# Kernel tuning notes

Hardware: AMD Instinct MI355X
Metric: run time of the kernel (lower is better)

The kernel has to match this reference:

```python
import jax, jax.numpy as jnp
import numpy as np

N, E, H, G = 50000, 500000, 64, 64


def _ln(x, g, b):
    m = jnp.mean(x, -1, keepdims=True)
    v = jnp.var(x, -1, keepdims=True)
    return (x - m) * jax.lax.rsqrt(v + 1e-5) * g + b


def _mlp_ln(x, w1, b1, w2, b2, g, be):
    # Linear -> ReLU -> (Dropout eval no-op) -> Linear -> LayerNorm
    h = jax.nn.relu(x @ w1 + b1)
    return _ln(h @ w2 + b2, g, be)


def setup_inputs() -> dict:
    key = jax.random.key(0)
    ks = jax.random.split(key, 24)
    w = lambda i, s: jax.random.normal(ks[i], s, dtype=jnp.float32) * 0.1
    z = lambda s: jnp.zeros(s, jnp.float32)
    o = lambda s: jnp.ones(s, jnp.float32)
    inp = {
        'x': jax.random.normal(ks[0], (N, 3), dtype=jnp.float32),
        'edge_index': jax.random.randint(ks[1], (2, E), 0, N),
        'edge_attr': jax.random.normal(ks[2], (E, 3), dtype=jnp.float32),
        'batch': jnp.sort(jax.random.randint(ks[3], (N,), 0, G)),
        'ne_w1': w(4, (3, H)), 'ne_b1': z((H,)), 'ne_w2': w(5, (H, H)), 'ne_b2': z((H,)), 'ne_g': o((H,)), 'ne_be': z((H,)),
        'ee_w1': w(6, (3, H)), 'ee_b1': z((H,)), 'ee_w2': w(7, (H, H)), 'ee_b2': z((H,)), 'ee_g': o((H,)), 'ee_be': z((H,)),
        'gin0_eps': z((1,)), 'gin0_w1': w(8, (H, H)), 'gin0_b1': z((H,)), 'gin0_w2': w(9, (H, H)), 'gin0_b2': z((H,)), 'gin0_g': o((H,)), 'gin0_be': z((H,)),
        'gin1_eps': z((1,)), 'gin1_w1': w(10, (H, H)), 'gin1_b1': z((H,)), 'gin1_w2': w(11, (H, H)), 'gin1_b2': z((H,)), 'gin1_g': o((H,)), 'gin1_be': z((H,)),
        'gp_w': w(12, (H, H)), 'gp_b': z((H,)), 'gp_g': o((H,)), 'gp_be': z((H,)),
        'ep_w1': w(13, (4 * H, 2 * H)), 'ep_b1': z((2 * H,)),
        'ep_w2': w(14, (2 * H, H)), 'ep_b2': z((H,)),
        'ep_w3': w(15, (H, 1)), 'ep_b3': z((1,)),
    }
    return inp


def reference(x, edge_index, edge_attr, batch,
              ne_w1, ne_b1, ne_w2, ne_b2, ne_g, ne_be,
              ee_w1, ee_b1, ee_w2, ee_b2, ee_g, ee_be,
              gin0_eps, gin0_w1, gin0_b1, gin0_w2, gin0_b2, gin0_g, gin0_be,
              gin1_eps, gin1_w1, gin1_b1, gin1_w2, gin1_b2, gin1_g, gin1_be,
              gp_w, gp_b, gp_g, gp_be,
              ep_w1, ep_b1, ep_w2, ep_b2, ep_w3, ep_b3):
    src, dst = edge_index[0], edge_index[1]
    # encoders
    h = _mlp_ln(x, ne_w1, ne_b1, ne_w2, ne_b2, ne_g, ne_be)            # [N, H]
    ef = _mlp_ln(edge_attr, ee_w1, ee_b1, ee_w2, ee_b2, ee_g, ee_be)   # [E, H]
    # GINEConv layer 0: mlp((1+eps)*x + scatter_add(relu(x_src + e)))
    msg = jax.nn.relu(h[src] + ef)
    aggr = jnp.zeros_like(h).at[dst].add(msg)
    h = _mlp_ln((1.0 + gin0_eps) * h + aggr, gin0_w1, gin0_b1, gin0_w2, gin0_b2, gin0_g, gin0_be)
    h = jax.nn.relu(h)  # inter-layer activation (dropout eval no-op)
    # GINEConv layer 1
    msg = jax.nn.relu(h[src] + ef)
    aggr = jnp.zeros_like(h).at[dst].add(msg)
    h = _mlp_ln((1.0 + gin1_eps) * h + aggr, gin1_w1, gin1_b1, gin1_w2, gin1_b2, gin1_g, gin1_be)
    # global mean pool over graphs
    seg = jax.ops.segment_sum(h, batch, num_segments=G)                            # [G, H]
    cnt = jax.ops.segment_sum(jnp.ones((h.shape[0], 1), h.dtype), batch, num_segments=G)
    gp = seg / jnp.maximum(cnt, 1.0)
    gf = _ln(jax.nn.relu(gp @ gp_w + gp_b), gp_g, gp_be)                           # [G, H]
    # edge predictor on [src | dst | global | edge] = [E, 4H]
    c = jnp.concatenate([h[src], h[dst], gf[batch[src]], ef], axis=-1)
    t = jnp.tanh(c @ ep_w1 + ep_b1)
    t = jnp.tanh(t @ ep_w2 + ep_b2)
    return jax.nn.sigmoid(t @ ep_w3 + ep_b3)  # [E, 1]
```

## Files before the change

### kernel.cpp

```cpp
#include <hip/hip_runtime.h>
#include <hip/hip_bf16.h>

typedef unsigned int uint;
typedef unsigned short ushort;
typedef __attribute__((ext_vector_type(8))) short short8;
typedef __attribute__((ext_vector_type(4))) float floatx4;

__device__ __forceinline__ float bf2f(ushort u) { return __uint_as_float(((uint)u) << 16); }
__device__ __forceinline__ ushort f2bf(float f) {
  uint u = __float_as_uint(f);
  u += 0x7fffu + ((u >> 16) & 1u);
  return (ushort)(u >> 16);
}
__device__ __forceinline__ uint pk2(float a, float b) {
  return (uint)f2bf(a) | ((uint)f2bf(b) << 16);
}
__device__ __forceinline__ float ldf(const void* p, long i, int m) {
  if (m) return bf2f(((const ushort*)p)[i]);
  return ((const float*)p)[i];
}
__device__ __forceinline__ int get_md(const uint* mdp) {
  return (mdp[0] == 0x3F800000u) ? 0 : 1;
}
__device__ __forceinline__ float fast_rcp(float x) { return __builtin_amdgcn_rcpf(x); }
__device__ __forceinline__ float tanh_fast(float x) {
  float e = __builtin_amdgcn_exp2f(2.8853900818f * x);
  return fmaf(-2.f, fast_rcp(1.f + e), 1.f);
}
__device__ __forceinline__ float sigmoid_fast(float x) {
  float e = __builtin_amdgcn_exp2f(-1.4426950409f * x);
  return fast_rcp(1.f + e);
}

__global__ __launch_bounds__(256) void k_enc_mfma(
    const void* __restrict__ in, int R,
    const void* __restrict__ w1, const void* __restrict__ b1,
    const ushort* __restrict__ w2sw_, const void* __restrict__ b2,
    const void* __restrict__ gam, const void* __restrict__ bet,
    ushort* __restrict__ outp, ushort* __restrict__ outp2,
    const int* __restrict__ epos, const uint* __restrict__ mdp)
{
  __shared__ float xs[64*3];
  __shared__ float w1s[192], b1s[64], b2s[64], gs[64], bs2[64];
  __shared__ __align__(16) ushort T_s[64 * 72];
  int md = get_md(mdp);
  int tid = threadIdx.x;
  long e0 = (long)blockIdx.x * 64;
  if (tid < 192) {
    w1s[tid] = ldf(w1, tid, md);
    int row = tid / 3, cc = tid - row*3;
    long e = e0 + row;
    xs[tid] = (e < R) ? ldf(in, e*3 + cc, md) : 0.f;
  }
  if (tid < 64) { b1s[tid] = ldf(b1, tid, md); b2s[tid] = ldf(b2, tid, md);
                  gs[tid] = ldf(gam, tid, md); bs2[tid] = ldf(bet, tid, md); }
  __syncthreads();
  int lane = tid & 63, wv = tid >> 6;
  int quad = lane >> 4, mm = lane & 15;
  float x0 = xs[(wv*16 + mm)*3 + 0];
  float x1 = xs[(wv*16 + mm)*3 + 1];
  float x2 = xs[(wv*16 + mm)*3 + 2];
  short8 af[2];
#pragma unroll
  for (int s = 0; s < 2; ++s) {
#pragma unroll
    for (int j = 0; j < 8; ++j) {
      int f = s*32 + quad*8 + j;
      float hv = fmaxf(b1s[f] + x0*w1s[f] + x1*w1s[64+f] + x2*w1s[128+f], 0.f);
      af[s][j] = (short)f2bf(hv);
    }
  }
  floatx4 acc[4] = {};
  const short8* Bp = (const short8*)w2sw_;
#pragma unroll
  for (int s = 0; s < 2; ++s) {
#pragma unroll
    for (int t = 0; t < 4; ++t) {
      short8 b = Bp[(s*4 + t)*64 + lane];
      acc[t] = __builtin_amdgcn_mfma_f32_16x16x32_bf16(af[s], b, acc[t], 0, 0, 0);
    }
  }
  float vv[4][4];
#pragma unroll
  for (int t = 0; t < 4; ++t) {
    float bb = b2s[mm + 16*t];
#pragma unroll
    for (int r = 0; r < 4; ++r) vv[t][r] = acc[t][r] + bb;
  }
  float mr[4], vr[4];
#pragma unroll
  for (int r = 0; r < 4; ++r) {
    float s = vv[0][r] + vv[1][r] + vv[2][r] + vv[3][r];
#pragma unroll
    for (int off = 1; off < 16; off <<= 1) s += __shfl_xor(s, off);
    mr[r] = s * 0.015625f;
    float q = 0.f;
#pragma unroll
    for (int t = 0; t < 4; ++t) { float d = vv[t][r] - mr[r]; q = fmaf(d, d, q); }
#pragma unroll
    for (int off = 1; off < 16; off <<= 1) q += __shfl_xor(q, off);
    vr[r] = rsqrtf(q * 0.015625f + 1e-5f);
  }
#pragma unroll
  for (int t = 0; t < 4; ++t) {
    int col = mm + 16*t;
    float g = gs[col], be = bs2[col];
#pragma unroll
    for (int r = 0; r < 4; ++r)
      T_s[(wv*16 + quad*4 + r)*72 + col] = f2bf((vv[t][r] - mr[r]) * vr[r] * g + be);
  }
  __syncthreads();
#pragma unroll
  for (int i = 0; i < 2; ++i) {
    int gi = tid + 256*i;
    int row = gi >> 3, c = gi & 7;
    long e = e0 + row;
    if (e < R) {
      uint4 v = *(const uint4*)&T_s[row*72 + c*8];
      ((uint4*)(outp + e*64))[c] = v;
      if (outp2)
        ((uint4*)(outp2 + (long)epos[e]*64))[c] = v;
    }
  }
}

__global__ __launch_bounds__(256) void k_swz(
    const void* __restrict__ w1, const void* __restrict__ w2,
    const void* __restrict__ w2e, const void* __restrict__ w2n,
    const void* __restrict__ gw10, const void* __restrict__ gw20,
    const void* __restrict__ gw11, const void* __restrict__ gw21,
    ushort* __restrict__ w1sw, ushort* __restrict__ w2sw,
    ushort* __restrict__ ew2sw, ushort* __restrict__ nw2sw,
    ushort* __restrict__ g0w1sw, ushort* __restrict__ g0w2sw,
    ushort* __restrict__ g1w1sw, ushort* __restrict__ g1w2sw,
    int* __restrict__ deg, float* __restrict__ gsum, int Nn,
    const uint* __restrict__ mdp)
{
  int md = get_md(mdp);
  int i = blockIdx.x * 256 + threadIdx.x;
  int nthr = gridDim.x * 256;
  for (int k = i; k < Nn; k += nthr) deg[k] = 0;
  for (int k = i; k < 64*64 + 64; k += nthr) gsum[k] = 0.f;
  if (i < 32768) {
    int q = i & 7, lane = (i >> 3) & 63, tt = (i >> 9) & 7, s = i >> 12;
    int k = s*32 + (lane >> 4)*8 + q, n = (lane & 15) + 16*tt;
    w1sw[i] = f2bf(ldf(w1, k*128 + n, md));
  }
  if (i < 8192) {
    int q = i & 7, lane = (i >> 3) & 63, tt = (i >> 9) & 3, s = i >> 11;
    int k = s*32 + (lane >> 4)*8 + q, n = (lane & 15) + 16*tt;
    int src = k*64 + n;
    w2sw[i]   = f2bf(ldf(w2,   src, md));
    ew2sw[i]  = f2bf(ldf(w2e,  src, md));
    nw2sw[i]  = f2bf(ldf(w2n,  src, md));
    g0w1sw[i] = f2bf(ldf(gw10, src, md));
    g0w2sw[i] = f2bf(ldf(gw20, src, md));
    g1w1sw[i] = f2bf(ldf(gw11, src, md));
    g1w2sw[i] = f2bf(ldf(gw21, src, md));
  }
}

__global__ __launch_bounds__(256) void k_deg(
    const int* __restrict__ ei, int* __restrict__ deg, int E_)
{
  int e = blockIdx.x * 256 + threadIdx.x;
  if (e < E_) atomicAdd(&deg[ei[E_ + e]], 1);
}

__global__ __launch_bounds__(256) void k_scan1(
    const int* __restrict__ deg, int* __restrict__ rs, int* __restrict__ bsum, int Nn)
{
  __shared__ int ls[256];
  int tid = threadIdx.x;
  int i = blockIdx.x * 256 + tid;
  int v = (i < Nn) ? deg[i] : 0;
  ls[tid] = v;
  __syncthreads();
  for (int off = 1; off < 256; off <<= 1) {
    int t = (tid >= off) ? ls[tid - off] : 0;
    __syncthreads();
    ls[tid] += t;
    __syncthreads();
  }
  if (i < Nn) rs[i] = ls[tid] - v;
  if (tid == 255) bsum[blockIdx.x] = ls[255];
}

__global__ __launch_bounds__(256) void k_scan2(
    int* __restrict__ bsum, int nb, int* __restrict__ rs, int Nn)
{
  __shared__ int ls[256];
  int tid = threadIdx.x;
  int chunk = (nb + 255) / 256;
  int c0 = tid * chunk, c1 = min(c0 + chunk, nb);
  int sum = 0;
  for (int i = c0; i < c1; ++i) sum += bsum[i];
  ls[tid] = sum;
  __syncthreads();
  for (int off = 1; off < 256; off <<= 1) {
    int t = (tid >= off) ? ls[tid - off] : 0;
    __syncthreads();
    ls[tid] += t;
    __syncthreads();
  }
  int run = ls[tid] - sum;
  for (int i = c0; i < c1; ++i) { int d = bsum[i]; bsum[i] = run; run += d; }
  if (tid == 255) rs[Nn] = ls[255];
}

__global__ __launch_bounds__(256) void k_scan3(
    int* __restrict__ rs, int* __restrict__ cur,
    const int* __restrict__ bsum, int Nn)
{
  int i = blockIdx.x * 256 + threadIdx.x;
  if (i < Nn) {
    int v = rs[i] + bsum[blockIdx.x];
    rs[i] = v;
    cur[i] = v;
  }
}

__global__ __launch_bounds__(256) void k_fill(
    const int* __restrict__ ei, int* __restrict__ cur,
    int2* __restrict__ ep, int* __restrict__ epos, int E_)
{
  int e = blockIdx.x * 256 + threadIdx.x;
  if (e < E_) {
    int s = ei[e];
    int d = ei[E_ + e];
    int p = atomicAdd(&cur[d], 1);
    ep[p] = make_int2(e, s);
    epos[e] = p;
  }
}

__global__ __launch_bounds__(256) void k_aggr(
    const ushort* __restrict__ hbu, const ushort* __restrict__ efp,
    const int2* __restrict__ ep, const int* __restrict__ rs,
    float* __restrict__ aggr, int Nn)
{
  int gw = (blockIdx.x * 256 + threadIdx.x) >> 6;
  int j = threadIdx.x & 63;
  if (gw >= Nn) return;
  int s0 = rs[gw], s1 = rs[gw + 1];
  float acc = 0.f;
  int idx = s0;
  for (; idx + 2 <= s1; idx += 2) {
    int2 a = ep[idx];
    int2 b = ep[idx + 1];
    float fA = bf2f(efp[(long)idx*64 + j]);
    float fB = bf2f(efp[(long)(idx+1)*64 + j]);
    float hA = bf2f(hbu[(long)a.y*64 + j]);
    float hB = bf2f(hbu[(long)b.y*64 + j]);
    acc += fmaxf(hA + fA, 0.f) + fmaxf(hB + fB, 0.f);
  }
  if (idx < s1) {
    int2 a = ep[idx];
    acc += fmaxf(bf2f(hbu[(long)a.y*64 + j]) + bf2f(efp[(long)idx*64 + j]), 0.f);
  }
  aggr[(long)gw*64 + j] = acc;
}

__global__ __launch_bounds__(256) void k_gine_mfma(
    const ushort* __restrict__ hbin, const float* __restrict__ aggr, int Nn,
    const void* __restrict__ epsp,
    const ushort* __restrict__ w1sw_, const void* __restrict__ b1,
    const ushort* __restrict__ w2sw_, const void* __restrict__ b2,
    const void* __restrict__ gam, const void* __restrict__ bet,
    ushort* __restrict__ hbout, int post_relu, const uint* __restrict__ mdp)
{
  __shared__ __align__(16) ushort Ws1[4096], Ws2[4096];
  __shared__ __align__(16) ushort T_s[64 * 72];
  __shared__ float b1s[64], b2s[64], gs[64], bs2[64];
  int md = get_md(mdp);
  int tid = threadIdx.x;
  {
    const uint4* p1 = (const uint4*)w1sw_;
    const uint4* p2 = (const uint4*)w2sw_;
    ((uint4*)Ws1)[tid] = p1[tid];
    ((uint4*)Ws1)[tid + 256] = p1[tid + 256];
    ((uint4*)Ws2)[tid] = p2[tid];
    ((uint4*)Ws2)[tid + 256] = p2[tid + 256];
  }
  if (tid < 64) { b1s[tid] = ldf(b1, tid, md); b2s[tid] = ldf(b2, tid, md);
                  gs[tid] = ldf(gam, tid, md); bs2[tid] = ldf(bet, tid, md); }
  float ope = 1.f + ldf(epsp, 0, md);
  int lane = tid & 63, wv = tid >> 6;
  int quad = lane >> 4, mm = lane & 15;
  long node = (long)blockIdx.x * 64 + wv*16 + mm;
  long nc = (node < Nn) ? node : (long)(Nn - 1);
  const ushort* hrow = hbin + nc*64;
  const float*  arow = aggr + nc*64;
  short8 af[2];
#pragma unroll
  for (int s = 0; s < 2; ++s) {
    int c = s*4 + quad;
    short8 hv = *(const short8*)(hrow + c*8);
    float4 a0 = *(const float4*)(arow + c*8);
    float4 a1 = *(const float4*)(arow + c*8 + 4);
    float uu[8];
    uu[0] = fmaf(bf2f((ushort)hv[0]), ope, a0.x);
    uu[1] = fmaf(bf2f((ushort)hv[1]), ope, a0.y);
    uu[2] = fmaf(bf2f((ushort)hv[2]), ope, a0.z);
    uu[3] = fmaf(bf2f((ushort)hv[3]), ope, a0.w);
    uu[4] = fmaf(bf2f((ushort)hv[4]), ope, a1.x);
    uu[5] = fmaf(bf2f((ushort)hv[5]), ope, a1.y);
    uu[6] = fmaf(bf2f((ushort)hv[6]), ope, a1.z);
    uu[7] = fmaf(bf2f((ushort)hv[7]), ope, a1.w);
#pragma unroll
    for (int j = 0; j < 8; ++j) af[s][j] = (short)f2bf(uu[j]);
  }
  __syncthreads();
  floatx4 acc[4] = {};
#pragma unroll
  for (int s = 0; s < 2; ++s) {
#pragma unroll
    for (int t = 0; t < 4; ++t) {
      short8 b = *(const short8*)&Ws1[((s*4 + t)*64 + lane)*8];
      acc[t] = __builtin_amdgcn_mfma_f32_16x16x32_bf16(af[s], b, acc[t], 0, 0, 0);
    }
  }
#pragma unroll
  for (int t = 0; t < 4; ++t) {
    int col = mm + 16*t;
    float bb = b1s[col];
#pragma unroll
    for (int r = 0; r < 4; ++r)
      T_s[(wv*16 + quad*4 + r)*72 + col] = f2bf(fmaxf(acc[t][r] + bb, 0.f));
  }
  __syncthreads();
  short8 af2[2];
#pragma unroll
  for (int s = 0; s < 2; ++s)
    af2[s] = *(const short8*)&T_s[(wv*16 + mm)*72 + s*32 + quad*8];
  floatx4 acc2[4] = {};
#pragma unroll
  for (int s = 0; s < 2; ++s) {
#pragma unroll
    for (int t = 0; t < 4; ++t) {
      short8 b = *(const short8*)&Ws2[((s*4 + t)*64 + lane)*8];
      acc2[t] = __builtin_amdgcn_mfma_f32_16x16x32_bf16(af2[s], b, acc2[t], 0, 0, 0);
    }
  }
  float vv[4][4];
#pragma unroll
  for (int t = 0; t < 4; ++t) {
    float bb = b2s[mm + 16*t];
#pragma unroll
    for (int r = 0; r < 4; ++r) vv[t][r] = acc2[t][r] + bb;
  }
  float mr[4], vr[4];
#pragma unroll
  for (int r = 0; r < 4; ++r) {
    float s = vv[0][r] + vv[1][r] + vv[2][r] + vv[3][r];
#pragma unroll
    for (int off = 1; off < 16; off <<= 1) s += __shfl_xor(s, off);
    mr[r] = s * 0.015625f;
    float q = 0.f;
#pragma unroll
    for (int t = 0; t < 4; ++t) { float d = vv[t][r] - mr[r]; q = fmaf(d, d, q); }
#pragma unroll
    for (int off = 1; off < 16; off <<= 1) q += __shfl_xor(q, off);
    vr[r] = rsqrtf(q * 0.015625f + 1e-5f);
  }
  __syncthreads();
#pragma unroll
  for (int t = 0; t < 4; ++t) {
    int col = mm + 16*t;
    float g = gs[col], be = bs2[col];
#pragma unroll
    for (int r = 0; r < 4; ++r) {
      float o = (vv[t][r] - mr[r]) * vr[r] * g + be;
      if (post_relu) o = fmaxf(o, 0.f);
      T_s[(wv*16 + quad*4 + r)*72 + col] = f2bf(o);
    }
  }
  __syncthreads();
#pragma unroll
  for (int i = 0; i < 2; ++i) {
    int gi = tid + 256*i;
    int row = gi >> 3, c = gi & 7;
    long n2 = (long)blockIdx.x * 64 + row;
    if (n2 < Nn)
      ((uint4*)(hbout + n2*64))[c] = *(const uint4*)&T_s[row*72 + c*8];
  }
}

__global__ __launch_bounds__(256) void k_pool_f(
    const ushort* __restrict__ hbu, const int* __restrict__ batch,
    float* __restrict__ gsum, float* __restrict__ gcnt, int Nn)
{
  int gw = (blockIdx.x * 256 + threadIdx.x) >> 6;
  int j = threadIdx.x & 63;
  long r0 = (long)gw * 64;
  if (r0 >= Nn) return;
  long rend = min(r0 + 64, (long)Nn);
  float acc = 0.f; int cur = batch[r0]; int run = 0;
  for (long r = r0; r < rend; ++r) {
    int g = batch[r];
    if (g != cur) {
      atomicAdd(&gsum[cur*64 + j], acc);
      if (j == 0) atomicAdd(&gcnt[cur], (float)run);
      acc = 0.f; run = 0; cur = g;
    }
    acc += bf2f(hbu[r*64 + j]);
    run++;
  }
  atomicAdd(&gsum[cur*64 + j], acc);
  if (j == 0) atomicAdd(&gcnt[cur], (float)run);
}

__global__ __launch_bounds__(64) void k_pool_fin_f(
    const float* __restrict__ gsum, const float* __restrict__ gcnt,
    const void* __restrict__ gpw, const void* __restrict__ gpb,
    const void* __restrict__ gpg, const void* __restrict__ gpbe,
    ushort* __restrict__ gfb, const uint* __restrict__ mdp)
{
  __shared__ float wgs[4096];
  __shared__ float us[64];
  int md = get_md(mdp);
  int j = threadIdx.x;
  int g = blockIdx.x;
  for (int i = j; i < 4096; i += 64) wgs[i] = ldf(gpw, i, md);
  float ic = 1.f / fmaxf(gcnt[g], 1.f);
  us[j] = gsum[g*64 + j] * ic;
  __syncthreads();
  float t = ldf(gpb, j, md);
#pragma unroll
  for (int k = 0; k < 64; ++k) t = fmaf(us[k], wgs[k*64 + j], t);
  t = fmaxf(t, 0.f);
  float m = t;
#pragma unroll
  for (int off = 1; off < 64; off <<= 1) m += __shfl_xor(m, off);
  m *= 0.015625f;
  float d = t - m;
  float v = d * d;
#pragma unroll
  for (int off = 1; off < 64; off <<= 1) v += __shfl_xor(v, off);
  float rs = rsqrtf(v * 0.015625f + 1e-5f);
  gfb[g*64 + j] = f2bf(d * rs * ldf(gpg, j, md) + ldf(gpbe, j, md));
}

__global__ __launch_bounds__(256) void k_pred_mfma(
    const ushort* __restrict__ hb, const ushort* __restrict__ efu,
    const ushort* __restrict__ gfb, const int* __restrict__ ei,
    const int* __restrict__ batch,
    const ushort* __restrict__ w1sw, const ushort* __restrict__ w2sw,
    const void* __restrict__ pb1, const void* __restrict__ pb2,
    const void* __restrict__ pw3, const void* __restrict__ pb3,
    void* __restrict__ out, int E_, const uint* __restrict__ mdp)
{
  __shared__ __align__(16) ushort Ws[8192];
  __shared__ __align__(16) ushort T_s[64 * 136];
  __shared__ float b1s[128], b2s[64], w3s[64];
  int md = get_md(mdp);
  int tid = threadIdx.x;
  if (tid < 128) b1s[tid] = ldf(pb1, tid, md);
  if (tid < 64) { b2s[tid] = ldf(pb2, tid, md); w3s[tid] = ldf(pw3, tid, md); }
  long e0 = (long)blockIdx.x * 64;
  int lane = tid & 63, wv = tid >> 6;
  int quad = lane >> 4, mm = lane & 15;
  long e = e0 + wv*16 + mm;
  if (e >= E_) e = E_ - 1;
  int si = ei[e];
  int di = ei[E_ + e];
  int gi = batch[si];
  const short8* hsrc = (const short8*)(hb  + (long)si*64);
  const short8* hdst = (const short8*)(hb  + (long)di*64);
  const short8* gsrc = (const short8*)(gfb + (long)gi*64);
  const short8* esrc = (const short8*)(efu + e*64);
  short8 af[8];
  af[0] = hsrc[quad]; af[1] = hsrc[4 + quad];
  af[2] = hdst[quad]; af[3] = hdst[4 + quad];
  af[4] = gsrc[quad]; af[5] = gsrc[4 + quad];
  af[6] = esrc[quad]; af[7] = esrc[4 + quad];
  floatx4 acc[8] = {};
  for (int q = 0; q < 4; ++q) {
    __syncthreads();
    const uint4* wp = (const uint4*)(w1sw + q*8192);
#pragma unroll
    for (int i = 0; i < 4; ++i)
      ((uint4*)Ws)[tid + 256*i] = wp[tid + 256*i];
    __syncthreads();
#pragma unroll
    for (int s4 = 0; s4 < 2; ++s4) {
      short8 a = af[q*2 + s4];
#pragma unroll
      for (int t = 0; t < 8; ++t) {
        short8 b = *(const short8*)&Ws[((s4*8 + t)*64 + lane)*8];
        acc[t] = __builtin_amdgcn_mfma_f32_16x16x32_bf16(a, b, acc[t], 0, 0, 0);
      }
    }
  }
#pragma unroll
  for (int t = 0; t < 8; ++t) {
    float bb = b1s[mm + 16*t];
#pragma unroll
    for (int r = 0; r < 4; ++r)
      T_s[(16*wv + quad*4 + r)*136 + mm + 16*t] = f2bf(tanh_fast(acc[t][r] + bb));
  }
  __syncthreads();
  {
    const uint4* wp2 = (const uint4*)w2sw;
#pragma unroll
    for (int i = 0; i < 4; ++i)
      ((uint4*)Ws)[tid + 256*i] = wp2[tid + 256*i];
  }
  __syncthreads();
  floatx4 acc2[4] = {};
#pragma unroll
  for (int s2 = 0; s2 < 4; ++s2) {
    short8 a = *(const short8*)&T_s[(16*wv + mm)*136 + s2*32 + quad*8];
#pragma unroll
    for (int t = 0; t < 4; ++t) {
      short8 b = *(const short8*)&Ws[((s2*4 + t)*64 + lane)*8];
      acc2[t] = __builtin_amdgcn_mfma_f32_16x16x32_bf16(a, b, acc2[t], 0, 0, 0);
    }
  }
  float p0 = 0.f, p1 = 0.f, p2 = 0.f, p3 = 0.f;
#pragma unroll
  for (int t = 0; t < 4; ++t) {
    int col = mm + 16*t;
    float bb = b2s[col], w3v = w3s[col];
    p0 = fmaf(tanh_fast(acc2[t][0] + bb), w3v, p0);
    p1 = fmaf(tanh_fast(acc2[t][1] + bb), w3v, p1);
    p2 = fmaf(tanh_fast(acc2[t][2] + bb), w3v, p2);
    p3 = fmaf(tanh_fast(acc2[t][3] + bb), w3v, p3);
  }
#pragma unroll
  for (int off = 1; off < 16; off <<= 1) {
    p0 += __shfl_xor(p0, off);
    p1 += __shfl_xor(p1, off);
    p2 += __shfl_xor(p2, off);
    p3 += __shfl_xor(p3, off);
  }
  if (mm == 0) {
    float b3 = ldf(pb3, 0, md);
    long eb = e0 + 16*wv + quad*4;
    float ps[4] = {p0, p1, p2, p3};
#pragma unroll
    for (int r = 0; r < 4; ++r) {
      if (eb + r < E_) {
        float sg = sigmoid_fast(ps[r] + b3);
        if (md) ((ushort*)out)[eb + r] = f2bf(sg);
        else    ((float*)out)[eb + r]  = sg;
      }
    }
  }
}

extern "C" void kernel_launch(void* const* d_in, const int* in_sizes, int n_in,
                              void* d_out, int out_size, void* d_ws, size_t ws_size,
                              hipStream_t stream)
{
  const void* x     = d_in[0];
  const int*  ei    = (const int*)d_in[1];
  const void* eattr = d_in[2];
  const int*  batch = (const int*)d_in[3];
  const void* ne_w1 = d_in[4];  const void* ne_b1 = d_in[5];
  const void* ne_w2 = d_in[6];  const void* ne_b2 = d_in[7];
  const void* ne_g  = d_in[8];  const void* ne_be = d_in[9];
  const void* ee_w1 = d_in[10]; const void* ee_b1 = d_in[11];
  const void* ee_w2 = d_in[12]; const void* ee_b2 = d_in[13];
  const void* ee_g  = d_in[14]; const void* ee_be = d_in[15];
  const void* g0_ep = d_in[16];
  const void* g0_w1 = d_in[17]; const void* g0_b1 = d_in[18];
  const void* g0_w2 = d_in[19]; const void* g0_b2 = d_in[20];
  const void* g0_g  = d_in[21]; const void* g0_be = d_in[22];
  const void* g1_ep = d_in[23];
  const void* g1_w1 = d_in[24]; const void* g1_b1 = d_in[25];
  const void* g1_w2 = d_in[26]; const void* g1_b2 = d_in[27];
  const void* g1_g  = d_in[28]; const void* g1_be = d_in[29];
  const void* gp_w  = d_in[30]; const void* gp_b  = d_in[31];
  const void* gp_g  = d_in[32]; const void* gp_be = d_in[33];
  const void* ep_w1 = d_in[34]; const void* ep_b1 = d_in[35];
  const void* ep_w2 = d_in[36]; const void* ep_b2 = d_in[37];
  const void* ep_w3 = d_in[38]; const void* ep_b3 = d_in[39];

  int N = in_sizes[3];
  int E = in_sizes[1] / 2;
  const uint* mdp = (const uint*)ne_g;

  char* ws = (char*)d_ws;
  size_t off = 0;
  auto alloc = [&](size_t bytes) { char* p = ws + off; off += (bytes + 255) & ~(size_t)255; return p; };
  ushort* hb     = (ushort*)alloc((size_t)N * 64 * 2);
  ushort* efu    = (ushort*)alloc((size_t)E * 64 * 2);
  ushort* efp    = (ushort*)alloc((size_t)E * 64 * 2);
  float*  aggr   = (float*) alloc((size_t)N * 64 * 4);
  float*  gsum   = (float*) alloc((64 * 64 + 64) * 4);
  float*  gcnt   = gsum + 64 * 64;
  ushort* gfb    = (ushort*)alloc(64 * 64 * 2);
  ushort* w1sw   = (ushort*)alloc(32768 * 2);
  ushort* w2sw   = (ushort*)alloc(8192 * 2);
  ushort* ew2sw  = (ushort*)alloc(8192 * 2);
  ushort* nw2sw  = (ushort*)alloc(8192 * 2);
  ushort* g0w1sw = (ushort*)alloc(8192 * 2);
  ushort* g0w2sw = (ushort*)alloc(8192 * 2);
  ushort* g1w1sw = (ushort*)alloc(8192 * 2);
  ushort* g1w2sw = (ushort*)alloc(8192 * 2);
  int*    deg    = (int*)   alloc((size_t)N * 4);
  int*    rs     = (int*)   alloc((size_t)(N + 1) * 4);
  int*    cur    = (int*)   alloc((size_t)N * 4);
  int2*   ep     = (int2*)  alloc((size_t)E * 8);
  int*    epos   = (int*)   alloc((size_t)E * 4);
  int*    bsum   = (int*)   alloc((size_t)((N + 255) / 256) * 4);
  (void)ws_size; (void)n_in; (void)out_size;

  int gN = (N + 255) / 256;
  int gE = (E + 255) / 256;
  int gE64 = (E + 63) / 64;
  int gN64 = (N + 63) / 64;
  int gAggr = (int)(((long)N * 64 + 255) / 256);
  int gPool = ((N + 63) / 64 + 3) / 4;

  k_swz<<<128, 256, 0, stream>>>(ep_w1, ep_w2, ee_w2, ne_w2, g0_w1, g0_w2, g1_w1, g1_w2,
                                 w1sw, w2sw, ew2sw, nw2sw,
                                 g0w1sw, g0w2sw, g1w1sw, g1w2sw,
                                 deg, gsum, N, mdp);
  k_deg<<<gE, 256, 0, stream>>>(ei, deg, E);
  k_scan1<<<gN, 256, 0, stream>>>(deg, rs, bsum, N);
  k_scan2<<<1, 256, 0, stream>>>(bsum, gN, rs, N);
  k_scan3<<<gN, 256, 0, stream>>>(rs, cur, bsum, N);
  k_fill<<<gE, 256, 0, stream>>>(ei, cur, ep, epos, E);
  k_enc_mfma<<<gN64, 256, 0, stream>>>(x, N, ne_w1, ne_b1, nw2sw, ne_b2, ne_g, ne_be,
                                       hb, (ushort*)nullptr, (const int*)nullptr, mdp);
  k_enc_mfma<<<gE64, 256, 0, stream>>>(eattr, E, ee_w1, ee_b1, ew2sw, ee_b2, ee_g, ee_be,
                                       efu, efp, epos, mdp);
  k_aggr<<<gAggr, 256, 0, stream>>>(hb, efp, ep, rs, aggr, N);
  k_gine_mfma<<<gN64, 256, 0, stream>>>(hb, aggr, N, g0_ep, g0w1sw, g0_b1, g0w2sw, g0_b2,
                                        g0_g, g0_be, hb, 1, mdp);
  k_aggr<<<gAggr, 256, 0, stream>>>(hb, efp, ep, rs, aggr, N);
  k_gine_mfma<<<gN64, 256, 0, stream>>>(hb, aggr, N, g1_ep, g1w1sw, g1_b1, g1w2sw, g1_b2,
                                        g1_g, g1_be, hb, 0, mdp);
  k_pool_f<<<gPool, 256, 0, stream>>>(hb, batch, gsum, gcnt, N);
  k_pool_fin_f<<<64, 64, 0, stream>>>(gsum, gcnt, gp_w, gp_b, gp_g, gp_be, gfb, mdp);
  k_pred_mfma<<<gE64, 256, 0, stream>>>(hb, efu, gfb, ei, batch, w1sw, w2sw,
                                        ep_b1, ep_b2, ep_w3, ep_b3, d_out, E, mdp);
}
```

Baseline: 456.9 us.

## Fuse GINE aggregation into MLP kernel, merge encoders, drop unpermuted edge copy

Gathers neighbor messages inside the GINE MLP kernel, with each wave summing 16 nodes into shared memory. This removes the separate aggregation kernel and its fp32 aggr round trip. The node and edge encoders become one launch, and the edge features are now written only in CSR-permuted order. The predictor reads edge features through epos, which adds an indirect gather. Ping-pong h buffers avoid in-place hazards. In exchange, each block does its 64-node aggregation serially per wave, which may leave less memory parallelism than the old one-wave-per-node aggregation.

```diff
diff --git a/kernel.cpp b/kernel.cpp
--- a/kernel.cpp
+++ b/kernel.cpp
@@ -32,20 +32,35 @@
   return fast_rcp(1.f + e);
 }
 
-__global__ __launch_bounds__(256) void k_enc_mfma(
-    const void* __restrict__ in, int R,
-    const void* __restrict__ w1, const void* __restrict__ b1,
-    const ushort* __restrict__ w2sw_, const void* __restrict__ b2,
-    const void* __restrict__ gam, const void* __restrict__ bet,
-    ushort* __restrict__ outp, ushort* __restrict__ outp2,
-    const int* __restrict__ epos, const uint* __restrict__ mdp)
+__global__ __launch_bounds__(256) void k_enc_dual(
+    int nblkN,
+    const void* __restrict__ inN, int Nn,
+    const void* __restrict__ nw1, const void* __restrict__ nb1,
+    const ushort* __restrict__ nw2sw_, const void* __restrict__ nb2,
+    const void* __restrict__ ngam, const void* __restrict__ nbet,
+    ushort* __restrict__ outN,
+    const void* __restrict__ inE, int E_,
+    const void* __restrict__ ew1, const void* __restrict__ eb1,
+    const ushort* __restrict__ ew2sw_, const void* __restrict__ eb2,
+    const void* __restrict__ egam, const void* __restrict__ ebet,
+    ushort* __restrict__ outE, const int* __restrict__ epos,
+    const uint* __restrict__ mdp)
 {
   __shared__ float xs[64*3];
   __shared__ float w1s[192], b1s[64], b2s[64], gs[64], bs2[64];
   __shared__ __align__(16) ushort T_s[64 * 72];
   int md = get_md(mdp);
   int tid = threadIdx.x;
-  long e0 = (long)blockIdx.x * 64;
+  bool isNode = (blockIdx.x < (uint)nblkN);
+  const void* in  = isNode ? inN : inE;
+  const void* w1  = isNode ? nw1 : ew1;
+  const void* b1  = isNode ? nb1 : eb1;
+  const ushort* w2sw_ = isNode ? nw2sw_ : ew2sw_;
+  const void* b2  = isNode ? nb2 : eb2;
+  const void* gam = isNode ? ngam : egam;
+  const void* bet = isNode ? nbet : ebet;
+  int R = isNode ? Nn : E_;
+  long e0 = isNode ? (long)blockIdx.x * 64 : (long)(blockIdx.x - nblkN) * 64;
   if (tid < 192) {
     w1s[tid] = ldf(w1, tid, md);
     int row = tid / 3, cc = tid - row*3;
@@ -117,9 +132,8 @@
     long e = e0 + row;
     if (e < R) {
       uint4 v = *(const uint4*)&T_s[row*72 + c*8];
-      ((uint4*)(outp + e*64))[c] = v;
-      if (outp2)
-        ((uint4*)(outp2 + (long)epos[e]*64))[c] = v;
+      if (isNode) ((uint4*)(outN + e*64))[c] = v;
+      else        ((uint4*)(outE + (long)epos[e]*64))[c] = v;
     }
   }
 }
@@ -234,43 +248,19 @@
   }
 }
 
-__global__ __launch_bounds__(256) void k_aggr(
-    const ushort* __restrict__ hbu, const ushort* __restrict__ efp,
-    const int2* __restrict__ ep, const int* __restrict__ rs,
-    float* __restrict__ aggr, int Nn)
-{
-  int gw = (blockIdx.x * 256 + threadIdx.x) >> 6;
-  int j = threadIdx.x & 63;
-  if (gw >= Nn) return;
-  int s0 = rs[gw], s1 = rs[gw + 1];
-  float acc = 0.f;
-  int idx = s0;
-  for (; idx + 2 <= s1; idx += 2) {
-    int2 a = ep[idx];
-    int2 b = ep[idx + 1];
-    float fA = bf2f(efp[(long)idx*64 + j]);
-    float fB = bf2f(efp[(long)(idx+1)*64 + j]);
-    float hA = bf2f(hbu[(long)a.y*64 + j]);
-    float hB = bf2f(hbu[(long)b.y*64 + j]);
-    acc += fmaxf(hA + fA, 0.f) + fmaxf(hB + fB, 0.f);
-  }
-  if (idx < s1) {
-    int2 a = ep[idx];
-    acc += fmaxf(bf2f(hbu[(long)a.y*64 + j]) + bf2f(efp[(long)idx*64 + j]), 0.f);
-  }
-  aggr[(long)gw*64 + j] = acc;
-}
-
-__global__ __launch_bounds__(256) void k_gine_mfma(
-    const ushort* __restrict__ hbin, const float* __restrict__ aggr, int Nn,
+__global__ __launch_bounds__(256) void k_gine_fused(
+    const ushort* __restrict__ hbin, ushort* __restrict__ hbout, int Nn,
+    const ushort* __restrict__ efp, const int2* __restrict__ ep,
+    const int* __restrict__ rs,
     const void* __restrict__ epsp,
     const ushort* __restrict__ w1sw_, const void* __restrict__ b1,
     const ushort* __restrict__ w2sw_, const void* __restrict__ b2,
     const void* __restrict__ gam, const void* __restrict__ bet,
-    ushort* __restrict__ hbout, int post_relu, const uint* __restrict__ mdp)
+    int post_relu, const uint* __restrict__ mdp)
 {
   __shared__ __align__(16) ushort Ws1[4096], Ws2[4096];
   __shared__ __align__(16) ushort T_s[64 * 72];
+  __shared__ float u_s[64 * 68];
   __shared__ float b1s[64], b2s[64], gs[64], bs2[64];
   int md = get_md(mdp);
   int tid = threadIdx.x;
@@ -287,37 +277,47 @@
   float ope = 1.f + ldf(epsp, 0, md);
   int lane = tid & 63, wv = tid >> 6;
   int quad = lane >> 4, mm = lane & 15;
-  long node = (long)blockIdx.x * 64 + wv*16 + mm;
-  long nc = (node < Nn) ? node : (long)(Nn - 1);
-  const ushort* hrow = hbin + nc*64;
-  const float*  arow = aggr + nc*64;
+  int j = lane;
+  for (int i = 0; i < 16; ++i) {
+    long node = (long)blockIdx.x * 64 + wv*16 + i;
+    float acc = 0.f, hv = 0.f;
+    if (node < Nn) {
+      hv = bf2f(hbin[node*64 + j]);
+      int s0 = rs[node], s1 = rs[node + 1];
+      int idx = s0;
+      for (; idx + 2 <= s1; idx += 2) {
+        int2 a = ep[idx];
+        int2 b = ep[idx + 1];
+        float fA = bf2f(efp[(long)idx*64 + j]);
+        float fB = bf2f(efp[(long)(idx+1)*64 + j]);
+        float hA = bf2f(hbin[(long)a.y*64 + j]);
+        float hB = bf2f(hbin[(long)b.y*64 + j]);
+        acc += fmaxf(hA + fA, 0.f) + fmaxf(hB + fB, 0.f);
+      }
+      if (idx < s1) {
+        int2 a = ep[idx];
+        acc += fmaxf(bf2f(hbin[(long)a.y*64 + j]) + bf2f(efp[(long)idx*64 + j]), 0.f);
+      }
+    }
+    u_s[(wv*16 + i)*68 + j] = fmaf(hv, ope, acc);
+  }
+  __syncthreads();
   short8 af[2];
 #pragma unroll
   for (int s = 0; s < 2; ++s) {
-    int c = s*4 + quad;
-    short8 hv = *(const short8*)(hrow + c*8);
-    float4 a0 = *(const float4*)(arow + c*8);
-    float4 a1 = *(const float4*)(arow + c*8 + 4);
-    float uu[8];
-    uu[0] = fmaf(bf2f((ushort)hv[0]), ope, a0.x);
-    uu[1] = fmaf(bf2f((ushort)hv[1]), ope, a0.y);
-    uu[2] = fmaf(bf2f((ushort)hv[2]), ope, a0.z);
-    uu[3] = fmaf(bf2f((ushort)hv[3]), ope, a0.w);
-    uu[4] = fmaf(bf2f((ushort)hv[4]), ope, a1.x);
-    uu[5] = fmaf(bf2f((ushort)hv[5]), ope, a1.y);
-    uu[6] = fmaf(bf2f((ushort)hv[6]), ope, a1.z);
-    uu[7] = fmaf(bf2f((ushort)hv[7]), ope, a1.w);
-#pragma unroll
-    for (int j = 0; j < 8; ++j) af[s][j] = (short)f2bf(uu[j]);
-  }
-  __syncthreads();
-  floatx4 acc[4] = {};
+#pragma unroll
+    for (int jj = 0; jj < 8; ++jj) {
+      int k = s*32 + quad*8 + jj;
+      af[s][jj] = (short)f2bf(u_s[(wv*16 + mm)*68 + k]);
+    }
+  }
+  floatx4 acc1[4] = {};
 #pragma unroll
   for (int s = 0; s < 2; ++s) {
 #pragma unroll
     for (int t = 0; t < 4; ++t) {
       short8 b = *(const short8*)&Ws1[((s*4 + t)*64 + lane)*8];
-      acc[t] = __builtin_amdgcn_mfma_f32_16x16x32_bf16(af[s], b, acc[t], 0, 0, 0);
+      acc1[t] = __builtin_amdgcn_mfma_f32_16x16x32_bf16(af[s], b, acc1[t], 0, 0, 0);
     }
   }
 #pragma unroll
@@ -326,9 +326,8 @@
     float bb = b1s[col];
 #pragma unroll
     for (int r = 0; r < 4; ++r)
-      T_s[(wv*16 + quad*4 + r)*72 + col] = f2bf(fmaxf(acc[t][r] + bb, 0.f));
-  }
-  __syncthreads();
+      T_s[(wv*16 + quad*4 + r)*72 + col] = f2bf(fmaxf(acc1[t][r] + bb, 0.f));
+  }
   short8 af2[2];
 #pragma unroll
   for (int s = 0; s < 2; ++s)
@@ -363,7 +362,6 @@
     for (int off = 1; off < 16; off <<= 1) q += __shfl_xor(q, off);
     vr[r] = rsqrtf(q * 0.015625f + 1e-5f);
   }
-  __syncthreads();
 #pragma unroll
   for (int t = 0; t < 4; ++t) {
     int col = mm + 16*t;
@@ -442,7 +440,8 @@
 }
 
 __global__ __launch_bounds__(256) void k_pred_mfma(
-    const ushort* __restrict__ hb, const ushort* __restrict__ efu,
+    const ushort* __restrict__ hb, const ushort* __restrict__ efp,
+    const int* __restrict__ epos,
     const ushort* __restrict__ gfb, const int* __restrict__ ei,
     const int* __restrict__ batch,
     const ushort* __restrict__ w1sw, const ushort* __restrict__ w2sw,
@@ -465,10 +464,11 @@
   int si = ei[e];
   int di = ei[E_ + e];
   int gi = batch[si];
+  int pe = epos[e];
   const short8* hsrc = (const short8*)(hb  + (long)si*64);
   const short8* hdst = (const short8*)(hb  + (long)di*64);
   const short8* gsrc = (const short8*)(gfb + (long)gi*64);
-  const short8* esrc = (const short8*)(efu + e*64);
+  const short8* esrc = (const short8*)(efp + (long)pe*64);
   short8 af[8];
   af[0] = hsrc[quad]; af[1] = hsrc[4 + quad];
   af[2] = hdst[quad]; af[3] = hdst[4 + quad];
@@ -584,10 +584,9 @@
   char* ws = (char*)d_ws;
   size_t off = 0;
   auto alloc = [&](size_t bytes) { char* p = ws + off; off += (bytes + 255) & ~(size_t)255; return p; };
-  ushort* hb     = (ushort*)alloc((size_t)N * 64 * 2);
-  ushort* efu    = (ushort*)alloc((size_t)E * 64 * 2);
+  ushort* hbA    = (ushort*)alloc((size_t)N * 64 * 2);
+  ushort* hbB    = (ushort*)alloc((size_t)N * 64 * 2);
   ushort* efp    = (ushort*)alloc((size_t)E * 64 * 2);
-  float*  aggr   = (float*) alloc((size_t)N * 64 * 4);
   float*  gsum   = (float*) alloc((64 * 64 + 64) * 4);
   float*  gcnt   = gsum + 64 * 64;
   ushort* gfb    = (ushort*)alloc(64 * 64 * 2);
@@ -611,7 +610,6 @@
   int gE = (E + 255) / 256;
   int gE64 = (E + 63) / 64;
   int gN64 = (N + 63) / 64;
-  int gAggr = (int)(((long)N * 64 + 255) / 256);
   int gPool = ((N + 63) / 64 + 3) / 4;
 
   k_swz<<<128, 256, 0, stream>>>(ep_w1, ep_w2, ee_w2, ne_w2, g0_w1, g0_w2, g1_w1, g1_w2,
@@ -623,18 +621,18 @@
   k_scan2<<<1, 256, 0, stream>>>(bsum, gN, rs, N);
   k_scan3<<<gN, 256, 0, stream>>>(rs, cur, bsum, N);
   k_fill<<<gE, 256, 0, stream>>>(ei, cur, ep, epos, E);
-  k_enc_mfma<<<gN64, 256, 0, stream>>>(x, N, ne_w1, ne_b1, nw2sw, ne_b2, ne_g, ne_be,
-                                       hb, (ushort*)nullptr, (const int*)nullptr, mdp);
-  k_enc_mfma<<<gE64, 256, 0, stream>>>(eattr, E, ee_w1, ee_b1, ew2sw, ee_b2, ee_g, ee_be,
-                                       efu, efp, epos, mdp);
-  k_aggr<<<gAggr, 256, 0, stream>>>(hb, efp, ep, rs, aggr, N);
-  k_gine_mfma<<<gN64, 256, 0, stream>>>(hb, aggr, N, g0_ep, g0w1sw, g0_b1, g0w2sw, g0_b2,
-                                        g0_g, g0_be, hb, 1, mdp);
-  k_aggr<<<gAggr, 256, 0, stream>>>(hb, efp, ep, rs, aggr, N);
-  k_gine_mfma<<<gN64, 256, 0, stream>>>(hb, aggr, N, g1_ep, g1w1sw, g1_b1, g1w2sw, g1_b2,
-                                        g1_g, g1_be, hb, 0, mdp);
-  k_pool_f<<<gPool, 256, 0, stream>>>(hb, batch, gsum, gcnt, N);
+  k_enc_dual<<<gN64 + gE64, 256, 0, stream>>>(
+      gN64,
+      x, N, ne_w1, ne_b1, nw2sw, ne_b2, ne_g, ne_be, hbA,
+      eattr, E, ee_w1, ee_b1, ew2sw, ee_b2, ee_g, ee_be, efp, epos, mdp);
+  k_gine_fused<<<gN64, 256, 0, stream>>>(hbA, hbB, N, efp, ep, rs,
+                                         g0_ep, g0w1sw, g0_b1, g0w2sw, g0_b2,
+                                         g0_g, g0_be, 1, mdp);
+  k_gine_fused<<<gN64, 256, 0, stream>>>(hbB, hbA, N, efp, ep, rs,
+                                         g1_ep, g1w1sw, g1_b1, g1w2sw, g1_b2,
+                                         g1_g, g1_be, 0, mdp);
+  k_pool_f<<<gPool, 256, 0, stream>>>(hbA, batch, gsum, gcnt, N);
   k_pool_fin_f<<<64, 64, 0, stream>>>(gsum, gcnt, gp_w, gp_b, gp_g, gp_be, gfb, mdp);
-  k_pred_mfma<<<gE64, 256, 0, stream>>>(hb, efu, gfb, ei, batch, w1sw, w2sw,
+  k_pred_mfma<<<gE64, 256, 0, stream>>>(hbA, efp, epos, gfb, ei, batch, w1sw, w2sw,
                                         ep_b1, ep_b2, ep_w3, ep_b3, d_out, E, mdp);
 }
```

After: 582.6 us. +27.5%, slower.
